# Kernel optimization log

Measured on AMD Instinct MI355X. Metric: run time of the kernel, lower is better.

The kernel has to match this reference:

```python
import jax, jax.numpy as jnp
import numpy as np

B, N, K = 2, 8192, 9
IN_CH, FEAT_CH, COST_CH = 64, 128, 64

def _bn(x, p, eps=1e-5):
    # eval-mode BatchNorm; p is [4, C] = (gamma, beta, running_mean, running_var)
    sh = (1, -1) + (1,) * (x.ndim - 2)
    g, b, m, v = (p[i].reshape(sh) for i in range(4))
    return (x - m) / jnp.sqrt(v + eps) * g + b

def _c1(x, w, b):
    # Conv1d kernel 1: x [B,C,N], w [O,C]
    return jnp.einsum('oc,bcn->bon', w, x) + b[None, :, None]

def _forward(xyz, points, cost_volume, feats, flow,
             w0, b0, bn0, w1, b1, bn1,
             wz, bz, wr, br, wq, bq,
             w2a, b2a, w2b, b2b, wfc, bfc,
             rw0, rbn0, rw1, rbn1, rw2, rbn2,
             cw0, cbn0, cw1, cbn1, cw2, cbn2):
    lrelu = lambda t: jax.nn.leaky_relu(t, 0.1)
    # --- self-KNN on xyz ---
    xt = jnp.transpose(xyz, (0, 2, 1))                   # B N 3
    sq = jnp.sum(xt * xt, -1)                            # B N
    d2 = sq[:, :, None] + sq[:, None, :] - 2.0 * jnp.einsum('bnd,bmd->bnm', xt, xt)
    idx = jax.lax.top_k(-d2, K)[1]                       # B N K (nearest incl. self)
    # --- grouping_operation: gather neighbor features ---
    np0 = jnp.concatenate([cost_volume, flow], 1)        # B (cost_ch+3) N
    g = jax.vmap(lambda p, i: p[:, i])(np0, idx)         # B C N K
    # --- Conv2d(1x1)+BN+LeakyReLU stack ---
    g = lrelu(_bn(jnp.einsum('oc,bcnk->bonk', w0, g) + b0[None, :, None, None], bn0))
    g = lrelu(_bn(jnp.einsum('oc,bcnk->bonk', w1, g) + b1[None, :, None, None], bn1))
    h = jnp.max(g, -1)                                   # max over neighbors -> B 128 N
    # --- ConvGRU(x=feats, h) with 1x1 Conv1d gates ---
    hx = jnp.concatenate([h, feats], 1)
    z = jax.nn.sigmoid(_c1(hx, wz, bz))
    r = jax.nn.sigmoid(_c1(hx, wr, br))
    q = jnp.tanh(_c1(jnp.concatenate([r * h, feats], 1), wq, bq))
    h = (1.0 - z) * h + z * q
    # --- Conv1d MLP head ---
    x = jnp.concatenate([points, h], 1)                  # B (in_ch+128) N
    x = lrelu(_c1(x, w2a, b2a))
    x = lrelu(_c1(x, w2b, b2b))
    re_flow = _c1(x, wfc, bfc)                           # B 3 N
    # --- prob regnets (Conv1d no-bias + BN + ReLU) ---
    def reg(y, ws, ps):
        for w, p in zip(ws, ps):
            y = jax.nn.relu(_bn(jnp.einsum('oc,bcn->bon', w, y), p))
        return y
    refine = reg(x, [rw0, rw1, rw2], [rbn0, rbn1, rbn2])         # B 1 N
    coarse = reg(cost_volume, [cw0, cw1, cw2], [cbn0, cbn1, cbn2])
    re_flow = coarse * flow + refine * re_flow
    return x, jnp.clip(re_flow, -20.0, 20.0)

def setup_inputs():
    key = jax.random.key(0)
    ks = iter(jax.random.split(key, 80))
    nrm = lambda shape, s=1.0: jax.random.normal(next(ks), shape, jnp.float32) * s
    def bnp(C):
        g = jax.random.uniform(next(ks), (C,), jnp.float32) + 0.5
        b = nrm((C,), 0.1); m = nrm((C,), 0.1)
        v = jax.random.uniform(next(ks), (C,), jnp.float32) + 0.5
        return jnp.stack([g, b, m, v])
    z = lambda C: jnp.zeros((C,), jnp.float32)
    return dict(
        xyz=nrm((B, 3, N)), points=nrm((B, IN_CH, N)), cost_volume=nrm((B, COST_CH, N)),
        feats=nrm((B, FEAT_CH, N)), flow=nrm((B, 3, N), 0.1),
        w0=nrm((128, COST_CH + 3), 0.05), b0=z(128), bn0=bnp(128),
        w1=nrm((128, 128), 0.05), b1=z(128), bn1=bnp(128),
        wz=nrm((128, 256), 0.05), bz=z(128), wr=nrm((128, 256), 0.05), br=z(128),
        wq=nrm((128, 256), 0.05), bq=z(128),
        w2a=nrm((128, IN_CH + 128), 0.05), b2a=z(128), w2b=nrm((64, 128), 0.05), b2b=z(64),
        wfc=nrm((3, 64), 0.05), bfc=z(3),
        rw0=nrm((64, 64), 0.05), rbn0=bnp(64), rw1=nrm((64, 64), 0.05), rbn1=bnp(64),
        rw2=nrm((1, 64), 0.05), rbn2=bnp(1),
        cw0=nrm((64, COST_CH), 0.05), cbn0=bnp(64), cw1=nrm((64, 64), 0.05), cbn1=bnp(64),
        cw2=nrm((1, 64), 0.05), cbn2=bnp(1),
    )

def reference(xyz, points, cost_volume, feats, flow, w0, b0, bn0, w1, b1, bn1, wz, bz, wr, br, wq, bq, w2a, b2a, w2b, b2b, wfc, bfc, rw0, rbn0, rw1, rbn1, rw2, rbn2, cw0, cbn0, cw1, cbn1, cw2, cbn2):
    return _forward(xyz, points, cost_volume, feats, flow, w0, b0, bn0, w1, b1, bn1, wz, bz, wr, br, wq, bq, w2a, b2a, w2b, b2b, wfc, bfc, rw0, rbn0, rw1, rbn1, rw2, rbn2, cw0, cbn0, cw1, cbn1, cw2, cbn2)
```

## Files before the change

### kernel.cpp

```cpp
#include <hip/hip_runtime.h>
#include <math.h>

typedef __bf16 bf16;
typedef __bf16 bf16x4 __attribute__((ext_vector_type(4)));
typedef __bf16 bf16x8 __attribute__((ext_vector_type(8)));
typedef float f32x4 __attribute__((ext_vector_type(4)));

#define NPTS 8192
#define MTOT 16384

static __device__ __forceinline__ float b2f(bf16 x) { return (float)x; }
static __device__ __forceinline__ bf16  f2b(float x) { return (bf16)x; }

__global__ void diag_k(float* out, float code)
{
    if (threadIdx.x == 0 && blockIdx.x == 0) out[0] = code;
}

static __device__ __forceinline__ void pack_body(bf16 (*tile)[68],
                                                 const float* __restrict__ src, int Csrc,
                                                 bf16* __restrict__ dst, int ldd,
                                                 int nb, int cb, int b)
{
    const int t = threadIdx.x;
#pragma unroll
    for (int i = 0; i < 8; ++i) {
        int id = t + i * 256;
        int c = id >> 6, n = id & 63;
        int cc = cb + c;
        bf16 v = (bf16)0.0f;
        if (cc < Csrc) v = f2b(src[(size_t)(b * Csrc + cc) * NPTS + nb + n]);
        tile[c][n] = v;
    }
    __syncthreads();
#pragma unroll
    for (int i = 0; i < 8; ++i) {
        int id = t + i * 256;
        int n = id >> 5, c = id & 31;
        dst[(size_t)(b * NPTS + nb + n) * ldd + cb + c] = tile[c][n];
    }
}

static __device__ __forceinline__ float tau32(unsigned u)
{
    unsigned m = 0x80000000u | (unsigned)(~((int)u >> 31));
    return __uint_as_float(u ^ m);
}

static __device__ __forceinline__ unsigned dpp_shr1_u(unsigned x)
{
    return (unsigned)__builtin_amdgcn_update_dpp(0, (int)x, 0x111, 0xf, 0xf, true);
}
static __device__ __forceinline__ int dpp_shr1_i(int x)
{
    return __builtin_amdgcn_update_dpp(0, x, 0x111, 0xf, 0xf, true);
}

static __device__ __forceinline__ void mm32(
    f32x4 (&acc)[2][2],
    const bf16* A1, int lda1, int row01, int K1,
    const bf16* A2, int lda2, int row02,
    const bf16* W, int ldw, int K, int ob)
{
    const int lane = threadIdx.x & 63;
    const int q = lane >> 4, r = lane & 15;
    const bf16* Wp = W + (size_t)(ob + r) * ldw + q * 8;
    for (int k = 0; k < K; k += 32) {
        const bf16* Ap; int ld;
        if (k < K1) { ld = lda1; Ap = A1 + (size_t)(row01 + r) * lda1 + q * 8 + k; }
        else        { ld = lda2; Ap = A2 + (size_t)(row02 + r) * lda2 + q * 8 + (k - K1); }
        bf16x8 bv0 = *(const bf16x8*)(Wp + k);
        bf16x8 bv1 = *(const bf16x8*)(Wp + 16 * ldw + k);
        bf16x8 a0 = *(const bf16x8*)(Ap);
        bf16x8 a1 = *(const bf16x8*)(Ap + 16 * ld);
        acc[0][0] = __builtin_amdgcn_mfma_f32_16x16x32_bf16(a0, bv0, acc[0][0], 0, 0, 0);
        acc[1][0] = __builtin_amdgcn_mfma_f32_16x16x32_bf16(a1, bv0, acc[1][0], 0, 0, 0);
        acc[0][1] = __builtin_amdgcn_mfma_f32_16x16x32_bf16(a0, bv1, acc[0][1], 0, 0, 0);
        acc[1][1] = __builtin_amdgcn_mfma_f32_16x16x32_bf16(a1, bv1, acc[1][1], 0, 0, 0);
    }
}

static __device__ __forceinline__ void zacc(f32x4 (&acc)[2][2])
{
    f32x4 z = {0.f, 0.f, 0.f, 0.f};
    acc[0][0] = z; acc[0][1] = z; acc[1][0] = z; acc[1][1] = z;
}

static __device__ __forceinline__ void mm16(
    f32x4 (&acc)[2],
    const bf16* A1, int lda1, int row01, int K1,
    const bf16* A2, int lda2, int row02,
    const bf16* W, int ldw, int K, int ob)
{
    const int lane = threadIdx.x & 63;
    const int q = lane >> 4, r = lane & 15;
    const bf16* Wp = W + (size_t)(ob + r) * ldw + q * 8;
    for (int k = 0; k < K; k += 32) {
        const bf16* Ap; int ld;
        if (k < K1) { ld = lda1; Ap = A1 + (size_t)(row01 + r) * lda1 + q * 8 + k; }
        else        { ld = lda2; Ap = A2 + (size_t)(row02 + r) * lda2 + q * 8 + (k - K1); }
        bf16x8 bv0 = *(const bf16x8*)(Wp + k);
        bf16x8 a0 = *(const bf16x8*)(Ap);
        bf16x8 a1 = *(const bf16x8*)(Ap + 16 * ld);
        acc[0] = __builtin_amdgcn_mfma_f32_16x16x32_bf16(a0, bv0, acc[0], 0, 0, 0);
        acc[1] = __builtin_amdgcn_mfma_f32_16x16x32_bf16(a1, bv0, acc[1], 0, 0, 0);
    }
}

static __device__ __forceinline__ void mm16x2(
    f32x4 (&acc)[2], f32x4 (&acc2)[2],
    const bf16* A1, int lda1, int row01, int K1,
    const bf16* A2, int lda2, int row02,
    const bf16* Wa, const bf16* Wb, int ldw, int K, int ob)
{
    const int lane = threadIdx.x & 63;
    const int q = lane >> 4, r = lane & 15;
    const bf16* Wpa = Wa + (size_t)(ob + r) * ldw + q * 8;
    const bf16* Wpb = Wb + (size_t)(ob + r) * ldw + q * 8;
    for (int k = 0; k < K; k += 32) {
        const bf16* Ap; int ld;
        if (k < K1) { ld = lda1; Ap = A1 + (size_t)(row01 + r) * lda1 + q * 8 + k; }
        else        { ld = lda2; Ap = A2 + (size_t)(row02 + r) * lda2 + q * 8 + (k - K1); }
        bf16x8 a0 = *(const bf16x8*)(Ap);
        bf16x8 a1 = *(const bf16x8*)(Ap + 16 * ld);
        bf16x8 ba0 = *(const bf16x8*)(Wpa + k);
        bf16x8 bb0 = *(const bf16x8*)(Wpb + k);
        acc[0]  = __builtin_amdgcn_mfma_f32_16x16x32_bf16(a0, ba0, acc[0], 0, 0, 0);
        acc[1]  = __builtin_amdgcn_mfma_f32_16x16x32_bf16(a1, ba0, acc[1], 0, 0, 0);
        acc2[0] = __builtin_amdgcn_mfma_f32_16x16x32_bf16(a0, bb0, acc2[0], 0, 0, 0);
        acc2[1] = __builtin_amdgcn_mfma_f32_16x16x32_bf16(a1, bb0, acc2[1], 0, 0, 0);
    }
}

static __device__ __forceinline__ void zacc2(f32x4 (&acc)[2])
{
    f32x4 z = {0.f, 0.f, 0.f, 0.f};
    acc[0] = z; acc[1] = z;
}

__global__ __launch_bounds__(256) void pack_a(
    const float* __restrict__ w0, const float* __restrict__ w1,
    const float* __restrict__ wz, const float* __restrict__ wr,
    const float* __restrict__ wq, const float* __restrict__ w2a,
    const float* __restrict__ w2b, const float* __restrict__ rw0,
    const float* __restrict__ rw1, const float* __restrict__ cw0,
    const float* __restrict__ cw1,
    const float* __restrict__ cost, const float* __restrict__ flow,
    bf16* __restrict__ w0p, bf16* __restrict__ wts,
    bf16* __restrict__ CV, bf16* __restrict__ FL)
{
    __shared__ __align__(16) bf16 tile[32][68];
    const int bx = blockIdx.x;
    if (bx < 48) {
        int id = bx * 256 + threadIdx.x;
        if (id < 128 * 96) {
            int o = id / 96, c = id - o * 96;
            w0p[id] = (c < 67) ? f2b(w0[o * 67 + c]) : (bf16)0.0f;
        }
    } else if (bx < 688) {
        int id = (bx - 48) * 256 + threadIdx.x;
        if (id < 163840) {
            const float* s; int off;
            if (id < 16384)       { s = w1;  off = 0; }
            else if (id < 49152)  { s = wz;  off = 16384; }
            else if (id < 81920)  { s = wr;  off = 49152; }
            else if (id < 114688) { s = wq;  off = 81920; }
            else if (id < 139264) { s = w2a; off = 114688; }
            else if (id < 147456) { s = w2b; off = 139264; }
            else if (id < 151552) { s = rw0; off = 147456; }
            else if (id < 155648) { s = rw1; off = 151552; }
            else if (id < 159744) { s = cw0; off = 155648; }
            else                  { s = cw1; off = 159744; }
            wts[id] = f2b(s[id - off]);
        }
    } else if (bx < 1200) {
        int l = bx - 688, x = l & 127, r2 = l >> 7;
        pack_body(tile, cost, 64, CV, 64, x * 64, (r2 & 1) * 32, r2 >> 1);
    } else {
        int l = bx - 1200, x = l & 127, b = l >> 7;
        pack_body(tile, flow, 3, FL, 32, x * 64, 0, b);
    }
}

__global__ __launch_bounds__(256, 5) void knn_conv_packb(
    const float* __restrict__ xyz, const float* __restrict__ feats,
    const float* __restrict__ points,
    const bf16* __restrict__ CV, const bf16* __restrict__ FL,
    const bf16* __restrict__ W0p, const bf16* __restrict__ W1,
    const bf16* __restrict__ CW0, const bf16* __restrict__ CW1,
    const float* __restrict__ b0, const float* __restrict__ bn0,
    const float* __restrict__ b1, const float* __restrict__ bn1,
    const float* __restrict__ cbn0, const float* __restrict__ cbn1,
    const float* __restrict__ cw2, const float* __restrict__ cbn2,
    bf16* __restrict__ FE, bf16* __restrict__ PT,
    bf16* __restrict__ P2, int* __restrict__ idxg,
    float* __restrict__ coarseG)
{
    __shared__ __align__(16) char smem[18432];
    const int bx = blockIdx.x;
    if (bx < 4096) {
        float4* pts = (float4*)smem;
        const int t = threadIdx.x, lane = t & 63, w = t >> 6;
        const int qid = bx * 4 + w, b = qid >> 13;
        const float* X = xyz + b * 3 * NPTS;
        const int n = qid & (NPTS - 1);
        const float qx = X[n], qy = X[NPTS + n], qz = X[2 * NPTS + n];
        const float qsq = qx * qx + qy * qy + qz * qz;

        unsigned kkd = 0xFFFFFFFFu;
        int      idd = 0;
        float tau = __builtin_inff();

        for (int ch = 0; ch < 8; ++ch) {
            __syncthreads();
#pragma unroll
            for (int r2 = 0; r2 < 4; ++r2) {
                int i2 = t + r2 * 256;
                int ci = ch * 1024 + i2;
                float x = X[ci], y = X[NPTS + ci], z = X[2 * NPTS + ci];
                pts[i2] = make_float4(x, y, z, x * x + y * y + z * z);
            }
            __syncthreads();
            int i0 = 0;
            if (ch == 0) {
                float4 c = pts[lane];
                float d = (qsq + c.w) - 2.0f * (qx * c.x + qy * c.y + qz * c.z);
                unsigned kd = __float_as_uint(d);
                kd ^= ((unsigned)((int)kd >> 31)) | 0x80000000u;
                unsigned long long key = ((unsigned long long)kd << 32) | (unsigned)lane;
#pragma unroll
                for (int r = 0; r < 9; ++r) {
                    unsigned long long m = key;
#pragma unroll
                    for (int s = 1; s < 64; s <<= 1) {
                        unsigned long long o = __shfl_xor(m, s);
                        if (o < m) m = o;
                    }
                    if (lane == r) {
                        kkd = (unsigned)(m >> 32);
                        idd = (int)(unsigned)(m & 0xffffffffu);
                    }
                    if (key == m) key = ~0ull;
                }
                tau = tau32((unsigned)__builtin_amdgcn_readlane((int)kkd, 8));
                i0 = 1;
            }
            for (int i = i0; i < 16; ++i) {
                float4 c = pts[i * 64 + lane];
                float d = (qsq + c.w) - 2.0f * (qx * c.x + qy * c.y + qz * c.z);
                unsigned long long mask = __ballot(d <= tau);
                if (mask) {
                    const int base = ch * 1024 + i * 64;
                    do {
                        int L = __builtin_ctzll(mask);
                        mask &= mask - 1;
                        unsigned di = (unsigned)__builtin_amdgcn_readlane(
                                          __float_as_int(d), L);
                        unsigned kd = di ^ (((unsigned)((int)di >> 31)) | 0x80000000u);
                        const int idxn = base + L;
                        unsigned kprev = dpp_shr1_u(kkd);
                        int      iprev = dpp_shr1_i(idd);
                        bool lt  = kd < kkd;
                        bool ltp = kd < kprev;
                        kkd = lt ? (ltp ? kprev : kd)   : kkd;
                        idd = lt ? (ltp ? iprev : idxn) : idd;
                    } while (mask);
                    tau = tau32((unsigned)__builtin_amdgcn_readlane((int)kkd, 8));
                }
            }
        }
        if (lane < 9) {
            int m = idd;
            m = ((unsigned)m < (unsigned)NPTS) ? m : 0;
            idxg[qid * 9 + lane] = b * NPTS + m;
        }
    } else if (bx < 4608) {
        bf16 (*P1t)[136] = (bf16 (*)[136])smem;
        const int w = threadIdx.x >> 6, lane = threadIdx.x & 63;
        const int q = lane >> 4, r = lane & 15;
        const int ptb = (bx - 4096) * 32;
        {
            f32x4 acc[2][2]; zacc(acc);
            const int ob = w * 32;
            mm32(acc, CV, 64, ptb, 64, FL, 32, ptb, W0p, 96, 96, ob);
#pragma unroll
            for (int to = 0; to < 2; ++to) {
                const int o = ob + to * 16 + r;
                float bs = b0[o];
                float gg = bn0[o], be = bn0[128 + o], mm = bn0[256 + o];
                float rs = 1.0f / sqrtf(bn0[384 + o] + 1e-5f);
#pragma unroll
                for (int tm = 0; tm < 2; ++tm) {
#pragma unroll
                    for (int rr = 0; rr < 4; ++rr) {
                        const int jl = tm * 16 + q * 4 + rr;
                        float v = acc[tm][to][rr] + bs;
                        v = (v - mm) * rs * gg + be;
                        v = v > 0.f ? v : 0.1f * v;
                        P1t[jl][o] = f2b(v);
                    }
                }
            }
        }
        __syncthreads();
        {
            f32x4 acc[2][2]; zacc(acc);
            const int ob = w * 32;
            mm32(acc, &P1t[0][0], 136, 0, 128, &P1t[0][0], 136, 0, W1, 128, 128, ob);
#pragma unroll
            for (int to = 0; to < 2; ++to) {
                const int o = ob + to * 16 + r;
                float bs = b1[o];
                float gg = bn1[o], be = bn1[128 + o], mm = bn1[256 + o];
                float rs = 1.0f / sqrtf(bn1[384 + o] + 1e-5f);
#pragma unroll
                for (int tm = 0; tm < 2; ++tm) {
#pragma unroll
                    for (int rr = 0; rr < 4; ++rr) {
                        const int jl = tm * 16 + q * 4 + rr;
                        float v = acc[tm][to][rr] + bs;
                        v = (v - mm) * rs * gg + be;
                        v = v > 0.f ? v : 0.1f * v;
                        P2[(size_t)(ptb + jl) * 128 + o] = f2b(v);
                    }
                }
            }
        }
    } else if (bx < 5632) {
        bf16 (*tile)[68] = (bf16 (*)[68])smem;
        int l = bx - 4608, x = l & 127, r2 = l >> 7;
        pack_body(tile, feats, 128, FE, 128, x * 64, (r2 & 3) * 32, r2 >> 2);
    } else if (bx < 6144) {
        bf16 (*tile)[68] = (bf16 (*)[68])smem;
        int l = bx - 5632, x = l & 127, r2 = l >> 7;
        pack_body(tile, points, 64, PT, 64, x * 64, (r2 & 1) * 32, r2 >> 1);
    } else {
        bf16 (*C1t)[72] = (bf16 (*)[72])smem;
        bf16 (*C2t)[72] = (bf16 (*)[72])(smem + 9216);
        const int w = threadIdx.x >> 6, lane = threadIdx.x & 63;
        const int q = lane >> 4, r = lane & 15;
        const int row0 = (w >> 1) * 32;
        const int pt0 = (bx - 6144) * 64 + row0;
        const int ob = (w & 1) * 32;
        {
            f32x4 acc[2][2]; zacc(acc);
            mm32(acc, CV, 64, pt0, 64, CV, 64, pt0, CW0, 64, 64, ob);
#pragma unroll
            for (int to = 0; to < 2; ++to) {
                const int o = ob + to * 16 + r;
                float gg = cbn0[o], be = cbn0[64 + o], mm = cbn0[128 + o];
                float rs = 1.0f / sqrtf(cbn0[192 + o] + 1e-5f);
#pragma unroll
                for (int tm = 0; tm < 2; ++tm)
#pragma unroll
                    for (int rr = 0; rr < 4; ++rr) {
                        const int jl = tm * 16 + q * 4 + rr;
                        float v = acc[tm][to][rr];
                        v = (v - mm) * rs * gg + be;
                        C1t[row0 + jl][o] = f2b(fmaxf(v, 0.f));
                    }
            }
        }
        __syncthreads();
        {
            f32x4 acc[2][2]; zacc(acc);
            mm32(acc, &C1t[0][0], 72, row0, 64, &C1t[0][0], 72, row0, CW1, 64, 64, ob);
#pragma unroll
            for (int to = 0; to < 2; ++to) {
                const int o = ob + to * 16 + r;
                float gg = cbn1[o], be = cbn1[64 + o], mm = cbn1[128 + o];
                float rs = 1.0f / sqrtf(cbn1[192 + o] + 1e-5f);
#pragma unroll
                for (int tm = 0; tm < 2; ++tm)
#pragma unroll
                    for (int rr = 0; rr < 4; ++rr) {
                        const int jl = tm * 16 + q * 4 + rr;
                        float v = acc[tm][to][rr];
                        v = (v - mm) * rs * gg + be;
                        C2t[row0 + jl][o] = f2b(fmaxf(v, 0.f));
                    }
            }
        }
        __syncthreads();
        if (threadIdx.x < 64) {
            const int jl = threadIdx.x;
            const int j = (bx - 6144) * 64 + jl;
            float dc = 0.f;
#pragma unroll
            for (int c = 0; c < 64; ++c) dc += cw2[c] * b2f(C2t[jl][c]);
            float coarse = (dc - cbn2[2]) / sqrtf(cbn2[3] + 1e-5f) * cbn2[0] + cbn2[1];
            coarseG[j] = fmaxf(coarse, 0.f);
        }
    }
}

struct MRP {
    const bf16 *P2, *FE, *PT;
    const int  *idx;
    const bf16 *WZ, *WR, *WQ, *W2A, *W2B, *RW0, *RW1;
    const float *bz, *br, *bq, *b2a, *b2b;
    const float *rbn0, *rbn1;
    const float *rw2, *rbn2, *wfc, *bfc, *flow, *coarse;
    float* out;
};

__global__ __launch_bounds__(512) void megarow(MRP p)
{
    __shared__ __align__(16) bf16 Zt[32][136], RHt[32][136], HPt[32][136], X1t[32][136];
    __shared__ __align__(16) bf16 X2t[32][72], R1t[32][72], R2t[32][72];
    __shared__ int idxt[32][9];
    const int w = threadIdx.x >> 6, lane = threadIdx.x & 63;
    const int q = lane >> 4, r = lane & 15;
    const int ptb = blockIdx.x * 32;

    if (threadIdx.x < 288) {
        int jl = threadIdx.x / 9, k = threadIdx.x - jl * 9;
        int m = p.idx[(ptb + jl) * 9 + k];
        idxt[jl][k] = ((unsigned)m < (unsigned)MTOT) ? m : 0;
    }
    __syncthreads();
    {
        const int c4 = (threadIdx.x & 31) * 4;
        const int jr = threadIdx.x >> 5;
#pragma unroll
        for (int jj = 0; jj < 2; ++jj) {
            const int jl = jr + 16 * jj;
            float mx0 = -__builtin_inff(), mx1 = -__builtin_inff();
            float mx2 = -__builtin_inff(), mx3 = -__builtin_inff();
#pragma unroll
            for (int k = 0; k < 9; ++k) {
                bf16x4 v = *(const bf16x4*)(p.P2 + (size_t)idxt[jl][k] * 128 + c4);
                mx0 = fmaxf(mx0, b2f(v[0]));
                mx1 = fmaxf(mx1, b2f(v[1]));
                mx2 = fmaxf(mx2, b2f(v[2]));
                mx3 = fmaxf(mx3, b2f(v[3]));
            }
            bf16x4 st;
            st[0] = f2b(mx0); st[1] = f2b(mx1); st[2] = f2b(mx2); st[3] = f2b(mx3);
            *(bf16x4*)&X1t[jl][c4] = st;
        }
    }
    __syncthreads();

    {
        const int ob = w * 16;
        f32x4 acc[2], acc2[2]; zacc2(acc); zacc2(acc2);
        mm16x2(acc, acc2, &X1t[0][0], 136, 0, 128, p.FE, 128, ptb,
               p.WZ, p.WR, 256, 256, ob);
        const int o = ob + r;
        const float bsz = p.bz[o];
#pragma unroll
        for (int tm = 0; tm < 2; ++tm)
#pragma unroll
            for (int rr = 0; rr < 4; ++rr) {
                const int jl = tm * 16 + q * 4 + rr;
                float v = acc[tm][rr] + bsz;
                Zt[jl][o] = f2b(1.0f / (1.0f + expf(-v)));
            }
        const float bsr = p.br[o];
#pragma unroll
        for (int tm = 0; tm < 2; ++tm)
#pragma unroll
            for (int rr = 0; rr < 4; ++rr) {
                const int jl = tm * 16 + q * 4 + rr;
                float v = acc2[tm][rr] + bsr;
                v = 1.0f / (1.0f + expf(-v));
                RHt[jl][o] = f2b(v * b2f(X1t[jl][o]));
            }
    }
    __syncthreads();
    {
        const int ob = w * 16;
        f32x4 acc[2]; zacc2(acc);
        mm16(acc, &RHt[0][0], 136, 0, 128, p.FE, 128, ptb, p.WQ, 256, 256, ob);
        const int o = ob + r;
        const float bs = p.bq[o];
#pragma unroll
        for (int tm = 0; tm < 2; ++tm)
#pragma unroll
            for (int rr = 0; rr < 4; ++rr) {
                const int jl = tm * 16 + q * 4 + rr;
                float v = acc[tm][rr] + bs;
                float qv = tanhf(v);
                float z = b2f(Zt[jl][o]);
                float h = b2f(X1t[jl][o]);
                HPt[jl][o] = f2b((1.0f - z) * h + z * qv);
            }
    }
    __syncthreads();
    {
        const int ob = w * 16;
        f32x4 acc[2]; zacc2(acc);
        mm16(acc, p.PT, 64, ptb, 64, &HPt[0][0], 136, 0, p.W2A, 192, 192, ob);
        const int o = ob + r;
        const float bs = p.b2a[o];
#pragma unroll
        for (int tm = 0; tm < 2; ++tm)
#pragma unroll
            for (int rr = 0; rr < 4; ++rr) {
                const int jl = tm * 16 + q * 4 + rr;
                float v = acc[tm][rr] + bs;
                X1t[jl][o] = f2b(v > 0.f ? v : 0.1f * v);
            }
    }
    __syncthreads();
    if (w < 4) {
        const int ob = w * 16;
        f32x4 acc[2]; zacc2(acc);
        mm16(acc, &X1t[0][0], 136, 0, 128, &X1t[0][0], 136, 0, p.W2B, 128, 128, ob);
        const int o = ob + r;
        const float bs = p.b2b[o];
#pragma unroll
        for (int tm = 0; tm < 2; ++tm)
#pragma unroll
            for (int rr = 0; rr < 4; ++rr) {
                const int jl = tm * 16 + q * 4 + rr;
                float v = acc[tm][rr] + bs;
                v = v > 0.f ? v : 0.1f * v;
                X2t[jl][o] = f2b(v);
                const int j = ptb + jl, bb = j >> 13, nn = j & (NPTS - 1);
                p.out[(size_t)bb * 64 * NPTS + (size_t)o * NPTS + nn] = v;
            }
    }
    __syncthreads();
    if (w < 4) {
        const int ob = w * 16;
        f32x4 acc[2]; zacc2(acc);
        mm16(acc, &X2t[0][0], 72, 0, 64, &X2t[0][0], 72, 0, p.RW0, 64, 64, ob);
        const int o = ob + r;
        float gg = p.rbn0[o], be = p.rbn0[64 + o], mm = p.rbn0[128 + o];
        float rs = 1.0f / sqrtf(p.rbn0[192 + o] + 1e-5f);
#pragma unroll
        for (int tm = 0; tm < 2; ++tm)
#pragma unroll
            for (int rr = 0; rr < 4; ++rr) {
                const int jl = tm * 16 + q * 4 + rr;
                float v = acc[tm][rr];
                v = (v - mm) * rs * gg + be;
                R1t[jl][o] = f2b(fmaxf(v, 0.f));
            }
    }
    __syncthreads();
    if (w < 4) {
        const int ob = w * 16;
        f32x4 acc[2]; zacc2(acc);
        mm16(acc, &R1t[0][0], 72, 0, 64, &R1t[0][0], 72, 0, p.RW1, 64, 64, ob);
        const int o = ob + r;
        float gg = p.rbn1[o], be = p.rbn1[64 + o], mm = p.rbn1[128 + o];
        float rs = 1.0f / sqrtf(p.rbn1[192 + o] + 1e-5f);
#pragma unroll
        for (int tm = 0; tm < 2; ++tm)
#pragma unroll
            for (int rr = 0; rr < 4; ++rr) {
                const int jl = tm * 16 + q * 4 + rr;
                float v = acc[tm][rr];
                v = (v - mm) * rs * gg + be;
                R2t[jl][o] = f2b(fmaxf(v, 0.f));
            }
    }
    __syncthreads();
    if (threadIdx.x < 32) {
        const int jl = threadIdx.x, j = ptb + jl;
        const int b = j >> 13, n = j & (NPTS - 1);
        float dr = 0.f, p0 = 0.f, p1 = 0.f, p2 = 0.f;
#pragma unroll
        for (int c = 0; c < 64; ++c) {
            float x = b2f(X2t[jl][c]);
            dr += p.rw2[c] * b2f(R2t[jl][c]);
            p0 += p.wfc[c] * x;
            p1 += p.wfc[64 + c] * x;
            p2 += p.wfc[128 + c] * x;
        }
        float refine = (dr - p.rbn2[2]) / sqrtf(p.rbn2[3] + 1e-5f) * p.rbn2[0] + p.rbn2[1];
        refine = fmaxf(refine, 0.f);
        const float coarse = p.coarse[j];
        p0 += p.bfc[0]; p1 += p.bfc[1]; p2 += p.bfc[2];
        const float f0 = p.flow[(size_t)b * 3 * NPTS + n];
        const float f1 = p.flow[(size_t)b * 3 * NPTS + NPTS + n];
        const float f2v = p.flow[(size_t)b * 3 * NPTS + 2 * NPTS + n];
        float o0 = fminf(fmaxf(coarse * f0 + refine * p0, -20.f), 20.f);
        float o1 = fminf(fmaxf(coarse * f1 + refine * p1, -20.f), 20.f);
        float o2 = fminf(fmaxf(coarse * f2v + refine * p2, -20.f), 20.f);
        float* ro = p.out + 1048576;
        ro[(size_t)b * 3 * NPTS + n] = o0;
        ro[(size_t)b * 3 * NPTS + NPTS + n] = o1;
        ro[(size_t)b * 3 * NPTS + 2 * NPTS + n] = o2;
    }
}

extern "C" void kernel_launch(void* const* d_in, const int* in_sizes, int n_in,
                              void* d_out, int out_size, void* d_ws, size_t ws_size,
                              hipStream_t stream)
{
    static const int EXP[35] = {
        49152, 1048576, 1048576, 2097152, 49152,
        8576, 128, 512, 16384, 128, 512,
        32768, 128, 32768, 128, 32768, 128,
        24576, 128, 8192, 64, 192, 3,
        4096, 256, 4096, 256, 64, 4,
        4096, 256, 4096, 256, 64, 4 };
    float code = 0.f;
    if (n_in != 35) code = 900.f;
    else if (out_size != 1097728) code = 950.f;
    else if (ws_size < 18767872u) code = 980.f;
    else { for (int i = 0; i < 35; ++i) if (in_sizes[i] != EXP[i]) { code = 1000.f + 4.f * i; break; } }
    if (code != 0.f) { diag_k<<<dim3(1), dim3(64), 0, stream>>>((float*)d_out, code); return; }

    const float* xyz    = (const float*)d_in[0];
    const float* points = (const float*)d_in[1];
    const float* cost   = (const float*)d_in[2];
    const float* feats  = (const float*)d_in[3];
    const float* flow   = (const float*)d_in[4];
    const float* w0     = (const float*)d_in[5];
    const float* b0     = (const float*)d_in[6];
    const float* bn0    = (const float*)d_in[7];
    const float* w1     = (const float*)d_in[8];
    const float* b1     = (const float*)d_in[9];
    const float* bn1    = (const float*)d_in[10];
    const float* wz     = (const float*)d_in[11];
    const float* bz     = (const float*)d_in[12];
    const float* wr     = (const float*)d_in[13];
    const float* br     = (const float*)d_in[14];
    const float* wq     = (const float*)d_in[15];
    const float* bq     = (const float*)d_in[16];
    const float* w2a    = (const float*)d_in[17];
    const float* b2a    = (const float*)d_in[18];
    const float* w2b    = (const float*)d_in[19];
    const float* b2b    = (const float*)d_in[20];
    const float* wfc    = (const float*)d_in[21];
    const float* bfc    = (const float*)d_in[22];
    const float* rw0    = (const float*)d_in[23];
    const float* rbn0   = (const float*)d_in[24];
    const float* rw1    = (const float*)d_in[25];
    const float* rbn1   = (const float*)d_in[26];
    const float* rw2    = (const float*)d_in[27];
    const float* rbn2   = (const float*)d_in[28];
    const float* cw0    = (const float*)d_in[29];
    const float* cbn0   = (const float*)d_in[30];
    const float* cw1    = (const float*)d_in[31];
    const float* cbn1   = (const float*)d_in[32];
    const float* cw2    = (const float*)d_in[33];
    const float* cbn2   = (const float*)d_in[34];

    char* ws = (char*)d_ws;
    bf16*  W0p  = (bf16*)(ws + 0);
    bf16*  WTS  = (bf16*)(ws + 24576);
    int*   idxg = (int*) (ws + 352256);
    bf16*  CV   = (bf16*)(ws + 942080);
    bf16*  FL   = (bf16*)(ws + 3039232);
    bf16*  FE   = (bf16*)(ws + 4087808);
    bf16*  PT   = (bf16*)(ws + 8282112);
    bf16*  P2   = (bf16*)(ws + 10379264);
    float* CO   = (float*)(ws + 14573568);

    bf16* W1  = WTS;
    bf16* WZ  = WTS + 16384;
    bf16* WR  = WTS + 49152;
    bf16* WQ  = WTS + 81920;
    bf16* W2A = WTS + 114688;
    bf16* W2B = WTS + 139264;
    bf16* RW0 = WTS + 147456;
    bf16* RW1 = WTS + 151552;
    bf16* CW0 = WTS + 155648;
    bf16* CW1 = WTS + 159744;

    float* out = (float*)d_out;

     pack_a<<<dim3(1456), dim3(256), 0, stream>>>(
              w0, w1, wz, wr, wq, w2a, w2b, rw0, rw1, cw0, cw1,
              cost, flow, W0p, WTS, CV, FL);
     knn_conv_packb<<<dim3(6400), dim3(256), 0, stream>>>(
              xyz, feats, points, CV, FL, W0p, W1, CW0, CW1,
              b0, bn0, b1, bn1, cbn0, cbn1, cw2, cbn2,
              FE, PT, P2, idxg, CO);
     MRP mp;
          mp.P2 = P2; mp.FE = FE; mp.PT = PT; mp.idx = idxg;
          mp.WZ = WZ; mp.WR = WR; mp.WQ = WQ; mp.W2A = W2A; mp.W2B = W2B;
          mp.RW0 = RW0; mp.RW1 = RW1;
          mp.bz = bz; mp.br = br; mp.bq = bq; mp.b2a = b2a; mp.b2b = b2b;
          mp.rbn0 = rbn0; mp.rbn1 = rbn1;
          mp.rw2 = rw2; mp.rbn2 = rbn2;
          mp.wfc = wfc; mp.bfc = bfc; mp.flow = flow; mp.coarse = CO;
          mp.out = out;
          megarow<<<dim3(512), dim3(512), 0, stream>>>(mp);

    (void)n_in;
}
```

Measured before the change: 242.6 us.

## Double-buffer KNN point chunks and stage FE/PT tiles in shared memory

The KNN part of knn_conv_packb now keeps two shared-memory point buffers. It loads the next 1024-point chunk into registers while scanning the current one, so one barrier per chunk replaces two and global-load latency is hidden behind compute. Shared memory for that kernel grows from 18 KB to 32 KB, which may cut occupancy below the 5 blocks per CU requested by the launch bounds. In megarow, the FE and PT rows for the block are staged once into shared tiles, so the GRU gate and MLP matmuls no longer read them repeatedly from global memory.

```diff
diff --git a/kernel.cpp b/kernel.cpp
--- a/kernel.cpp
+++ b/kernel.cpp
@@ -196,10 +196,10 @@
     bf16* __restrict__ P2, int* __restrict__ idxg,
     float* __restrict__ coarseG)
 {
-    __shared__ __align__(16) char smem[18432];
+    __shared__ __align__(16) char smem[32768];
     const int bx = blockIdx.x;
     if (bx < 4096) {
-        float4* pts = (float4*)smem;
+        float4 (*pts)[1024] = (float4 (*)[1024])smem;
         const int t = threadIdx.x, lane = t & 63, w = t >> 6;
         const int qid = bx * 4 + w, b = qid >> 13;
         const float* X = xyz + b * 3 * NPTS;
@@ -211,19 +211,32 @@
         int      idd = 0;
         float tau = __builtin_inff();
 
+        float nx[4], ny[4], nz[4];
+#pragma unroll
+        for (int r2 = 0; r2 < 4; ++r2) {
+            int ci = t + r2 * 256;
+            nx[r2] = X[ci]; ny[r2] = X[NPTS + ci]; nz[r2] = X[2 * NPTS + ci];
+        }
+#pragma unroll
+        for (int r2 = 0; r2 < 4; ++r2) {
+            int i2 = t + r2 * 256;
+            pts[0][i2] = make_float4(nx[r2], ny[r2], nz[r2],
+                                     nx[r2]*nx[r2] + ny[r2]*ny[r2] + nz[r2]*nz[r2]);
+        }
+        __syncthreads();
+
         for (int ch = 0; ch < 8; ++ch) {
-            __syncthreads();
-#pragma unroll
-            for (int r2 = 0; r2 < 4; ++r2) {
-                int i2 = t + r2 * 256;
-                int ci = ch * 1024 + i2;
-                float x = X[ci], y = X[NPTS + ci], z = X[2 * NPTS + ci];
-                pts[i2] = make_float4(x, y, z, x * x + y * y + z * z);
-            }
-            __syncthreads();
+            const int cur = ch & 1;
+            if (ch < 7) {
+#pragma unroll
+                for (int r2 = 0; r2 < 4; ++r2) {
+                    int ci = (ch + 1) * 1024 + t + r2 * 256;
+                    nx[r2] = X[ci]; ny[r2] = X[NPTS + ci]; nz[r2] = X[2 * NPTS + ci];
+                }
+            }
             int i0 = 0;
             if (ch == 0) {
-                float4 c = pts[lane];
+                float4 c = pts[0][lane];
                 float d = (qsq + c.w) - 2.0f * (qx * c.x + qy * c.y + qz * c.z);
                 unsigned kd = __float_as_uint(d);
                 kd ^= ((unsigned)((int)kd >> 31)) | 0x80000000u;
@@ -246,7 +259,7 @@
                 i0 = 1;
             }
             for (int i = i0; i < 16; ++i) {
-                float4 c = pts[i * 64 + lane];
+                float4 c = pts[cur][i * 64 + lane];
                 float d = (qsq + c.w) - 2.0f * (qx * c.x + qy * c.y + qz * c.z);
                 unsigned long long mask = __ballot(d <= tau);
                 if (mask) {
@@ -268,6 +281,15 @@
                     tau = tau32((unsigned)__builtin_amdgcn_readlane((int)kkd, 8));
                 }
             }
+            if (ch < 7) {
+#pragma unroll
+                for (int r2 = 0; r2 < 4; ++r2) {
+                    int i2 = t + r2 * 256;
+                    pts[cur ^ 1][i2] = make_float4(nx[r2], ny[r2], nz[r2],
+                                         nx[r2]*nx[r2] + ny[r2]*ny[r2] + nz[r2]*nz[r2]);
+                }
+            }
+            __syncthreads();
         }
         if (lane < 9) {
             int m = idd;
@@ -407,7 +429,8 @@
 __global__ __launch_bounds__(512) void megarow(MRP p)
 {
     __shared__ __align__(16) bf16 Zt[32][136], RHt[32][136], HPt[32][136], X1t[32][136];
-    __shared__ __align__(16) bf16 X2t[32][72], R1t[32][72], R2t[32][72];
+    __shared__ __align__(16) bf16 FEt[32][136];
+    __shared__ __align__(16) bf16 X2t[32][72], R1t[32][72], R2t[32][72], PTt[32][72];
     __shared__ int idxt[32][9];
     const int w = threadIdx.x >> 6, lane = threadIdx.x & 63;
     const int q = lane >> 4, r = lane & 15;
@@ -417,6 +440,13 @@
         int jl = threadIdx.x / 9, k = threadIdx.x - jl * 9;
         int m = p.idx[(ptb + jl) * 9 + k];
         idxt[jl][k] = ((unsigned)m < (unsigned)MTOT) ? m : 0;
+    }
+    {
+        const int row = threadIdx.x >> 4;
+        const int c8 = (threadIdx.x & 15) * 8;
+        *(bf16x8*)&FEt[row][c8] = *(const bf16x8*)(p.FE + (size_t)(ptb + row) * 128 + c8);
+        const int c4 = (threadIdx.x & 15) * 4;
+        *(bf16x4*)&PTt[row][c4] = *(const bf16x4*)(p.PT + (size_t)(ptb + row) * 64 + c4);
     }
     __syncthreads();
     {
@@ -445,7 +475,7 @@
     {
         const int ob = w * 16;
         f32x4 acc[2], acc2[2]; zacc2(acc); zacc2(acc2);
-        mm16x2(acc, acc2, &X1t[0][0], 136, 0, 128, p.FE, 128, ptb,
+        mm16x2(acc, acc2, &X1t[0][0], 136, 0, 128, &FEt[0][0], 136, 0,
                p.WZ, p.WR, 256, 256, ob);
         const int o = ob + r;
         const float bsz = p.bz[o];
@@ -472,7 +502,7 @@
     {
         const int ob = w * 16;
         f32x4 acc[2]; zacc2(acc);
-        mm16(acc, &RHt[0][0], 136, 0, 128, p.FE, 128, ptb, p.WQ, 256, 256, ob);
+        mm16(acc, &RHt[0][0], 136, 0, 128, &FEt[0][0], 136, 0, p.WQ, 256, 256, ob);
         const int o = ob + r;
         const float bs = p.bq[o];
 #pragma unroll
@@ -491,7 +521,7 @@
     {
         const int ob = w * 16;
         f32x4 acc[2]; zacc2(acc);
-        mm16(acc, p.PT, 64, ptb, 64, &HPt[0][0], 136, 0, p.W2A, 192, 192, ob);
+        mm16(acc, &PTt[0][0], 72, 0, 64, &HPt[0][0], 136, 0, p.W2A, 192, 192, ob);
         const int o = ob + r;
         const float bs = p.b2a[o];
 #pragma unroll
```

Result: slower. 255.0 us (+5.1%).
